# Kernel tuning notes

Measured on AMD Instinct MI355X. Metric: run time of the kernel, lower is better.

## Reference

```python
import jax, jax.numpy as jnp
import numpy as np

B, H, S, D = 2, 16, 2048, 64

def setup_inputs() -> dict:
    key = jax.random.key(0)
    kq, kk, kv = jax.random.split(key, 3)
    Q = jax.random.normal(kq, (B, H, S, D), dtype=jnp.float32)
    K = jax.random.normal(kk, (B, H, S, D), dtype=jnp.float32)
    V = jax.random.normal(kv, (B, H, S, D), dtype=jnp.float32)
    # causal mask, broadcastable over batch and heads
    mask = jnp.tril(jnp.ones((S, S), dtype=bool))[None, None, :, :]
    return {"Q": Q, "K": K, "V": V, "mask": mask}

def reference(Q, K, V, mask):
    # scores: [B,H,S,S]
    scores = jnp.einsum('bhqd,bhkd->bhqk', Q, K)
    # original applies mask (-inf) BEFORE scaling; -inf/scale == -inf so math matches
    scores = jnp.where(mask, scores, -jnp.inf)
    scores = scores / jnp.sqrt(jnp.float32(K.shape[-1]))
    attn = jax.nn.softmax(scores, axis=-1)
    return jnp.einsum('bhqk,bhkd->bhqd', attn, V)
```

## Files before the change

kernel.cpp:

```cpp
#include <hip/hip_runtime.h>

#define SEQ 2048
#define HD  64

typedef __bf16 bf16x8 __attribute__((ext_vector_type(8)));
typedef __bf16 bf16x4 __attribute__((ext_vector_type(4)));
typedef float  f32x4  __attribute__((ext_vector_type(4)));
typedef float  f32x16 __attribute__((ext_vector_type(16)));

#define C1 0.18033688011111772f
#define C2 8.656170245333781f

__global__ __launch_bounds__(256, 2) void attn_fwd(
    const float* __restrict__ Q,
    const float* __restrict__ K,
    const float* __restrict__ V,
    float* __restrict__ O)
{
    __shared__ __bf16 Kb[64][64];
    __shared__ __bf16 Vt[64][64];
    __shared__ __bf16 Pw[4][32][72];

    const int tid  = threadIdx.x;
    const int wave = tid >> 6;
    const int lane = tid & 63;
    const int n    = lane & 31;
    const int p    = lane >> 5;

    const int x  = blockIdx.x;
    const int bh = x & 31;
    const int t  = x >> 5;
    const int half  = wave >> 1;
    const int strip = wave & 1;
    const int myTq  = half ? (31 - t) : t;
    const int q0    = myTq * 64 + strip * 32;
    const int my_nt  = myTq + 1;
    const int blk_nt = 32 - t;

    const float* __restrict__ Qh = Q + (size_t)bh * SEQ * HD;
    const float* __restrict__ Kh = K + (size_t)bh * SEQ * HD;
    const float* __restrict__ Vh = V + (size_t)bh * SEQ * HD;
    float* __restrict__       Oh = O + (size_t)bh * SEQ * HD;

    bf16x8 qf[4];
    {
        const float* qrow = Qh + (size_t)(q0 + n) * HD;
        #pragma unroll
        for (int c = 0; c < 4; ++c) {
            f32x4 a = *(const f32x4*)(qrow + 16 * c + 8 * p);
            f32x4 b = *(const f32x4*)(qrow + 16 * c + 8 * p + 4);
            #pragma unroll
            for (int j = 0; j < 4; ++j) {
                qf[c][j]     = (__bf16)a[j];
                qf[c][4 + j] = (__bf16)b[j];
            }
        }
    }

    bf16x8 ones;
    #pragma unroll
    for (int j = 0; j < 8; ++j) ones[j] = (__bf16)1.0f;

    f32x16 o_acc[2] = {};
    f32x16 l_acc = {};

    const int kk_s = tid >> 2;
    const int q_s  = tid & 3;
    const int swk  = (kk_s >> 1) & 7;
    const int L_s  = tid & 31;
    const int R_s  = tid >> 5;
    const int swv  = R_s ^ (L_s & 7);
    const int swf  = (n >> 1) & 7;

    f32x4  kpre[4];
    float2 vpre[8];
    {
        const float* kp = Kh + (size_t)kk_s * HD + q_s * 16;
        #pragma unroll
        for (int i = 0; i < 4; ++i) kpre[i] = *(const f32x4*)(kp + 4 * i);
        const float* vp = Vh + (size_t)(8 * R_s) * HD + 2 * L_s;
        #pragma unroll
        for (int i = 0; i < 8; ++i) vpre[i] = *(const float2*)(vp + (size_t)i * HD);
    }

    for (int s = 0; s < blk_nt; ++s) {
        __syncthreads();

        {
            bf16x8 w0, w1;
            #pragma unroll
            for (int j = 0; j < 4; ++j) {
                w0[j] = (__bf16)kpre[0][j]; w0[4 + j] = (__bf16)kpre[1][j];
                w1[j] = (__bf16)kpre[2][j]; w1[4 + j] = (__bf16)kpre[3][j];
            }
            *(bf16x8*)&Kb[kk_s][((2 * q_s)     ^ swk) * 8] = w0;
            *(bf16x8*)&Kb[kk_s][((2 * q_s + 1) ^ swk) * 8] = w1;

            bf16x8 v0, v1;
            #pragma unroll
            for (int i = 0; i < 8; ++i) {
                v0[i] = (__bf16)vpre[i].x;
                v1[i] = (__bf16)vpre[i].y;
            }
            *(bf16x8*)&Vt[2 * L_s][swv * 8]     = v0;
            *(bf16x8*)&Vt[2 * L_s + 1][swv * 8] = v1;
        }

        if (s + 1 < blk_nt) {
            const int k1 = (s + 1) * 64;
            const float* kp = Kh + (size_t)(k1 + kk_s) * HD + q_s * 16;
            #pragma unroll
            for (int i = 0; i < 4; ++i) kpre[i] = *(const f32x4*)(kp + 4 * i);
            const float* vp = Vh + (size_t)(k1 + 8 * R_s) * HD + 2 * L_s;
            #pragma unroll
            for (int i = 0; i < 8; ++i) vpre[i] = *(const float2*)(vp + (size_t)i * HD);
        }

        __syncthreads();

        if (s < my_nt) {
            f32x16 sT[2] = {};
            #pragma unroll
            for (int g = 0; g < 2; ++g) {
                const __bf16* krow = &Kb[32 * g + n][0];
                #pragma unroll
                for (int c = 0; c < 4; ++c) {
                    bf16x8 kf = *(const bf16x8*)(krow + (((2 * c + p) ^ swf) * 8));
                    sT[g] = __builtin_amdgcn_mfma_f32_32x32x16_bf16(kf, qf[c], sT[g], 0, 0, 0);
                }
            }

            const bool diag = (s == myTq);
            const int qcol = strip * 32 + n;
            #pragma unroll
            for (int g = 0; g < 2; ++g) {
                #pragma unroll
                for (int r1 = 0; r1 < 4; ++r1) {
                    bf16x4 pk;
                    #pragma unroll
                    for (int r0 = 0; r0 < 4; ++r0) {
                        float pv = __builtin_amdgcn_exp2f(fmaf(sT[g][r0 + 4 * r1], C1, -C2));
                        if (diag) {
                            const int kk = 32 * g + 8 * r1 + 4 * p + r0;
                            pv = (kk <= qcol) ? pv : 0.0f;
                        }
                        pk[r0] = (__bf16)pv;
                    }
                    *(bf16x4*)&Pw[wave][n][32 * g + 8 * r1 + 4 * p] = pk;
                }
            }

            bf16x8 pf[4];
            #pragma unroll
            for (int c = 0; c < 4; ++c)
                pf[c] = *(const bf16x8*)&Pw[wave][n][16 * c + 8 * p];

            #pragma unroll
            for (int c = 0; c < 4; ++c) {
                #pragma unroll
                for (int g = 0; g < 2; ++g) {
                    bf16x8 vf = *(const bf16x8*)&Vt[32 * g + n][(((2 * c + p) ^ swf) * 8)];
                    o_acc[g] = __builtin_amdgcn_mfma_f32_32x32x16_bf16(pf[c], vf, o_acc[g], 0, 0, 0);
                }
                l_acc = __builtin_amdgcn_mfma_f32_32x32x16_bf16(pf[c], ones, l_acc, 0, 0, 0);
            }
        }
    }

    #pragma unroll
    for (int r = 0; r < 16; ++r) {
        const int ql = (r & 3) + 8 * (r >> 2) + 4 * p;
        const float inv = 1.0f / l_acc[r];
        const size_t row = (size_t)(q0 + ql) * HD;
        Oh[row + n]      = o_acc[0][r] * inv;
        Oh[row + 32 + n] = o_acc[1][r] * inv;
    }
}

extern "C" void kernel_launch(void* const* d_in, const int* in_sizes, int n_in,
                              void* d_out, int out_size, void* d_ws, size_t ws_size,
                              hipStream_t stream) {
    const float* Q = (const float*)d_in[0];
    const float* K = (const float*)d_in[1];
    const float* V = (const float*)d_in[2];
    float* O = (float*)d_out;

    dim3 grid(512);
    dim3 block(256);
    attn_fwd<<<grid, block, 0, stream>>>(Q, K, V, O);
}
```

Measured before the change: 134.9 us.

## Split causal key range across wave pairs and merge partial outputs in shared memory

Each block now handles a single 64-row query tile, giving 1024 blocks, and its two wave pairs split the key range in half with 32-key tiles. The partial outputs and row sums are combined through shared memory at the end. The softmax scale is folded into Q, and the fixed -C2 offset is removed from the exponent, which was a constant shift with no running max. Row sums now use VALU adds instead of an extra MFMA against a ones vector, and occupancy is raised to 4 blocks per CU. Dropping the offset raises the risk of exp overflow for large scores, and the final merge adds shared-memory traffic and synchronization.

```diff
diff --git a/kernel.cpp b/kernel.cpp
--- a/kernel.cpp
+++ b/kernel.cpp
@@ -2,40 +2,40 @@
 
 #define SEQ 2048
 #define HD  64
+#define SCALE 0.18033688011111772f
 
 typedef __bf16 bf16x8 __attribute__((ext_vector_type(8)));
 typedef __bf16 bf16x4 __attribute__((ext_vector_type(4)));
 typedef float  f32x4  __attribute__((ext_vector_type(4)));
 typedef float  f32x16 __attribute__((ext_vector_type(16)));
 
-#define C1 0.18033688011111772f
-#define C2 8.656170245333781f
-
-__global__ __launch_bounds__(256, 2) void attn_fwd(
+__global__ __launch_bounds__(256, 4) void attn_fwd(
     const float* __restrict__ Q,
     const float* __restrict__ K,
     const float* __restrict__ V,
     float* __restrict__ O)
 {
-    __shared__ __bf16 Kb[64][64];
-    __shared__ __bf16 Vt[64][64];
-    __shared__ __bf16 Pw[4][32][72];
-
-    const int tid  = threadIdx.x;
-    const int wave = tid >> 6;
-    const int lane = tid & 63;
-    const int n    = lane & 31;
-    const int p    = lane >> 5;
+    __shared__ __align__(16) unsigned char smem[26624];
+    #define KBp(kh,key,c8) ((__bf16*)(smem +         (((kh)<<12) + ((key)<<7) + ((c8)<<4))))
+    #define VTp(kh,r,c8)   ((__bf16*)(smem +  8192 + (((kh)<<12) + ((r)<<6)   + ((c8)<<4))))
+    #define PWp(w,n,koff)  ((__bf16*)(smem + 16384 + ((w)*2560 + (n)*80 + ((koff)<<1))))
+
+    const int tid   = threadIdx.x;
+    const int wave  = tid >> 6;
+    const int lane  = tid & 63;
+    const int n     = lane & 31;
+    const int p     = lane >> 5;
+    const int strip = wave & 1;
+    const int kh    = wave >> 1;
 
     const int x  = blockIdx.x;
     const int bh = x & 31;
-    const int t  = x >> 5;
-    const int half  = wave >> 1;
-    const int strip = wave & 1;
-    const int myTq  = half ? (31 - t) : t;
-    const int q0    = myTq * 64 + strip * 32;
-    const int my_nt  = myTq + 1;
-    const int blk_nt = 32 - t;
+    const int s  = x >> 5;
+    const int q  = (s & 16) ? (31 - (s & 15)) : s;
+
+    const int q0    = q * 64 + strip * 32;
+    const int iters = q + 1;
+    const int tS0   = kh * (q + 1);
 
     const float* __restrict__ Qh = Q + (size_t)bh * SEQ * HD;
     const float* __restrict__ Kh = K + (size_t)bh * SEQ * HD;
@@ -51,129 +51,144 @@
             f32x4 b = *(const f32x4*)(qrow + 16 * c + 8 * p + 4);
             #pragma unroll
             for (int j = 0; j < 4; ++j) {
-                qf[c][j]     = (__bf16)a[j];
-                qf[c][4 + j] = (__bf16)b[j];
-            }
-        }
-    }
-
-    bf16x8 ones;
-    #pragma unroll
-    for (int j = 0; j < 8; ++j) ones[j] = (__bf16)1.0f;
-
-    f32x16 o_acc[2] = {};
-    f32x16 l_acc = {};
-
-    const int kk_s = tid >> 2;
-    const int q_s  = tid & 3;
-    const int swk  = (kk_s >> 1) & 7;
-    const int L_s  = tid & 31;
-    const int R_s  = tid >> 5;
-    const int swv  = R_s ^ (L_s & 7);
-    const int swf  = (n >> 1) & 7;
-
-    f32x4  kpre[4];
-    float2 vpre[8];
+                qf[c][j]     = (__bf16)(a[j] * SCALE);
+                qf[c][4 + j] = (__bf16)(b[j] * SCALE);
+            }
+        }
+    }
+
+    f32x16 oT[2] = {};
+    float  l_own = 0.f;
+
+    const int local = tid & 127;
+    const int key_s = local >> 2;
+    const int dgi   = local & 3;
+    const int Ls    = local & 31;
+    const int ko    = local >> 5;
+    const int swk   = key_s & 7;
+    const int swv   = Ls & 3;
+
+    const float* kbase = Kh + (size_t)key_s * HD + dgi * 16;
+    const float* vbase = Vh + (size_t)(ko * 8) * HD + 2 * Ls;
+
+    f32x4  kst[4];
+    float2 vst[8];
     {
-        const float* kp = Kh + (size_t)kk_s * HD + q_s * 16;
-        #pragma unroll
-        for (int i = 0; i < 4; ++i) kpre[i] = *(const f32x4*)(kp + 4 * i);
-        const float* vp = Vh + (size_t)(8 * R_s) * HD + 2 * L_s;
-        #pragma unroll
-        for (int i = 0; i < 8; ++i) vpre[i] = *(const float2*)(vp + (size_t)i * HD);
-    }
-
-    for (int s = 0; s < blk_nt; ++s) {
+        const float* kp = kbase + (size_t)(32 * tS0) * HD;
+        #pragma unroll
+        for (int i = 0; i < 4; ++i) kst[i] = *(const f32x4*)(kp + 4 * i);
+        const float* vp = vbase + (size_t)(32 * tS0) * HD;
+        #pragma unroll
+        for (int i = 0; i < 8; ++i) vst[i] = *(const float2*)(vp + (size_t)i * HD);
+    }
+
+    for (int i = 0; i < iters; ++i) {
         __syncthreads();
 
         {
             bf16x8 w0, w1;
             #pragma unroll
             for (int j = 0; j < 4; ++j) {
-                w0[j] = (__bf16)kpre[0][j]; w0[4 + j] = (__bf16)kpre[1][j];
-                w1[j] = (__bf16)kpre[2][j]; w1[4 + j] = (__bf16)kpre[3][j];
-            }
-            *(bf16x8*)&Kb[kk_s][((2 * q_s)     ^ swk) * 8] = w0;
-            *(bf16x8*)&Kb[kk_s][((2 * q_s + 1) ^ swk) * 8] = w1;
+                w0[j] = (__bf16)kst[0][j]; w0[4 + j] = (__bf16)kst[1][j];
+                w1[j] = (__bf16)kst[2][j]; w1[4 + j] = (__bf16)kst[3][j];
+            }
+            *(bf16x8*)KBp(kh, key_s, (2 * dgi)     ^ swk) = w0;
+            *(bf16x8*)KBp(kh, key_s, (2 * dgi + 1) ^ swk) = w1;
 
             bf16x8 v0, v1;
             #pragma unroll
-            for (int i = 0; i < 8; ++i) {
-                v0[i] = (__bf16)vpre[i].x;
-                v1[i] = (__bf16)vpre[i].y;
-            }
-            *(bf16x8*)&Vt[2 * L_s][swv * 8]     = v0;
-            *(bf16x8*)&Vt[2 * L_s + 1][swv * 8] = v1;
-        }
-
-        if (s + 1 < blk_nt) {
-            const int k1 = (s + 1) * 64;
-            const float* kp = Kh + (size_t)(k1 + kk_s) * HD + q_s * 16;
-            #pragma unroll
-            for (int i = 0; i < 4; ++i) kpre[i] = *(const f32x4*)(kp + 4 * i);
-            const float* vp = Vh + (size_t)(k1 + 8 * R_s) * HD + 2 * L_s;
-            #pragma unroll
-            for (int i = 0; i < 8; ++i) vpre[i] = *(const float2*)(vp + (size_t)i * HD);
+            for (int j = 0; j < 8; ++j) { v0[j] = (__bf16)vst[j].x; v1[j] = (__bf16)vst[j].y; }
+            *(bf16x8*)VTp(kh, 2 * Ls,     ko ^ swv) = v0;
+            *(bf16x8*)VTp(kh, 2 * Ls + 1, ko ^ swv) = v1;
+        }
+
+        if (i + 1 < iters) {
+            const size_t off = (size_t)(32 * (tS0 + i + 1)) * HD;
+            const float* kp = kbase + off;
+            #pragma unroll
+            for (int j = 0; j < 4; ++j) kst[j] = *(const f32x4*)(kp + 4 * j);
+            const float* vp = vbase + off;
+            #pragma unroll
+            for (int j = 0; j < 8; ++j) vst[j] = *(const float2*)(vp + (size_t)j * HD);
         }
 
         __syncthreads();
 
-        if (s < my_nt) {
-            f32x16 sT[2] = {};
-            #pragma unroll
-            for (int g = 0; g < 2; ++g) {
-                const __bf16* krow = &Kb[32 * g + n][0];
+        if (!kh || (i < q + strip)) {
+            f32x16 sT = {};
+            #pragma unroll
+            for (int cc = 0; cc < 4; ++cc) {
+                bf16x8 kf = *(const bf16x8*)KBp(kh, n, (2 * cc + p) ^ (n & 7));
+                sT = __builtin_amdgcn_mfma_f32_32x32x16_bf16(kf, qf[cc], sT, 0, 0, 0);
+            }
+
+            const int  T    = tS0 + i;
+            const bool diag = (T == 2 * q + strip);
+
+            float pv[16];
+            float ts = 0.f;
+            #pragma unroll
+            for (int r = 0; r < 16; ++r) {
+                float pe = __builtin_amdgcn_exp2f(sT[r]);
+                if (diag) {
+                    const int kk = (r & 3) + 8 * (r >> 2) + 4 * p;
+                    pe = (kk <= n) ? pe : 0.f;
+                }
+                pv[r] = pe;
+                ts += pe;
+            }
+            l_own += ts;
+
+            #pragma unroll
+            for (int m = 0; m < 4; ++m) {
+                bf16x4 pk;
                 #pragma unroll
-                for (int c = 0; c < 4; ++c) {
-                    bf16x8 kf = *(const bf16x8*)(krow + (((2 * c + p) ^ swf) * 8));
-                    sT[g] = __builtin_amdgcn_mfma_f32_32x32x16_bf16(kf, qf[c], sT[g], 0, 0, 0);
+                for (int j = 0; j < 4; ++j) pk[j] = (__bf16)pv[4 * m + j];
+                *(bf16x4*)PWp(wave, n, 8 * m + 4 * p) = pk;
+            }
+            bf16x8 pf0 = *(const bf16x8*)PWp(wave, n, 8 * p);
+            bf16x8 pf1 = *(const bf16x8*)PWp(wave, n, 16 + 8 * p);
+
+            const int swn = (n >> 1) & 3;
+            #pragma unroll
+            for (int dg = 0; dg < 2; ++dg) {
+                bf16x8 vf0 = *(const bf16x8*)VTp(kh, 32 * dg + n, p ^ swn);
+                bf16x8 vf1 = *(const bf16x8*)VTp(kh, 32 * dg + n, (2 + p) ^ swn);
+                oT[dg] = __builtin_amdgcn_mfma_f32_32x32x16_bf16(vf0, pf0, oT[dg], 0, 0, 0);
+                oT[dg] = __builtin_amdgcn_mfma_f32_32x32x16_bf16(vf1, pf1, oT[dg], 0, 0, 0);
+            }
+        }
+    }
+
+    __syncthreads();
+    float* Os = (float*)smem;
+    const int cb = strip * 2112;
+    float l_part = l_own + __shfl_xor(l_own, 32, 64);
+
+    if (kh == 1) {
+        #pragma unroll
+        for (int dg = 0; dg < 2; ++dg)
+            #pragma unroll
+            for (int r = 0; r < 16; ++r)
+                Os[cb + (dg * 16 + r) * 64 + lane] = oT[dg][r];
+        Os[cb + 2048 + lane] = l_part;
+    }
+    __syncthreads();
+    if (kh == 0) {
+        const float linv = 1.0f / (l_part + Os[cb + 2048 + lane]);
+        #pragma unroll
+        for (int dg = 0; dg < 2; ++dg) {
+            #pragma unroll
+            for (int u = 0; u < 4; ++u) {
+                f32x4 o;
+                #pragma unroll
+                for (int j = 0; j < 4; ++j) {
+                    const int r = 4 * u + j;
+                    o[j] = (oT[dg][r] + Os[cb + (dg * 16 + r) * 64 + lane]) * linv;
                 }
-            }
-
-            const bool diag = (s == myTq);
-            const int qcol = strip * 32 + n;
-            #pragma unroll
-            for (int g = 0; g < 2; ++g) {
-                #pragma unroll
-                for (int r1 = 0; r1 < 4; ++r1) {
-                    bf16x4 pk;
-                    #pragma unroll
-                    for (int r0 = 0; r0 < 4; ++r0) {
-                        float pv = __builtin_amdgcn_exp2f(fmaf(sT[g][r0 + 4 * r1], C1, -C2));
-                        if (diag) {
-                            const int kk = 32 * g + 8 * r1 + 4 * p + r0;
-                            pv = (kk <= qcol) ? pv : 0.0f;
-                        }
-                        pk[r0] = (__bf16)pv;
-                    }
-                    *(bf16x4*)&Pw[wave][n][32 * g + 8 * r1 + 4 * p] = pk;
-                }
-            }
-
-            bf16x8 pf[4];
-            #pragma unroll
-            for (int c = 0; c < 4; ++c)
-                pf[c] = *(const bf16x8*)&Pw[wave][n][16 * c + 8 * p];
-
-            #pragma unroll
-            for (int c = 0; c < 4; ++c) {
-                #pragma unroll
-                for (int g = 0; g < 2; ++g) {
-                    bf16x8 vf = *(const bf16x8*)&Vt[32 * g + n][(((2 * c + p) ^ swf) * 8)];
-                    o_acc[g] = __builtin_amdgcn_mfma_f32_32x32x16_bf16(pf[c], vf, o_acc[g], 0, 0, 0);
-                }
-                l_acc = __builtin_amdgcn_mfma_f32_32x32x16_bf16(pf[c], ones, l_acc, 0, 0, 0);
-            }
-        }
-    }
-
-    #pragma unroll
-    for (int r = 0; r < 16; ++r) {
-        const int ql = (r & 3) + 8 * (r >> 2) + 4 * p;
-        const float inv = 1.0f / l_acc[r];
-        const size_t row = (size_t)(q0 + ql) * HD;
-        Oh[row + n]      = o_acc[0][r] * inv;
-        Oh[row + 32 + n] = o_acc[1][r] * inv;
+                *(f32x4*)&Oh[(size_t)(q0 + n) * HD + dg * 32 + u * 8 + 4 * p] = o;
+            }
+        }
     }
 }
 
@@ -185,7 +200,7 @@
     const float* V = (const float*)d_in[2];
     float* O = (float*)d_out;
 
-    dim3 grid(512);
+    dim3 grid(1024);
     dim3 block(256);
     attn_fwd<<<grid, block, 0, stream>>>(Q, K, V, O);
 }
```

Measured after the change: 132.7 us. About the same (-1.7%).
